# Kernel tuning notes

Measured on AMD Instinct MI355X. Metric: run time of the kernel, lower is better.

The kernel has to match this reference:

```python
import jax, jax.numpy as jnp
import numpy as np

H = 512          # hidden_dim
AA = 21          # aa_num
NF = 6165        # num_features
B, N = 4, 2048   # graphs per batch, nodes per graph
LAMB = 1.0
OUT = 2


def gcn(x, adj, W, b):
    # Kipf GCN with self-loops on a (weighted) dense adjacency [B,n,n].
    n = adj.shape[-1]
    A = adj + jnp.eye(n, dtype=adj.dtype)
    d = jnp.sum(A, axis=-1)
    dinv = jax.lax.rsqrt(jnp.maximum(d, 1e-12))
    xw = x @ W                              # [B,n,Hout]
    msg = dinv[..., :, None] * (A @ (dinv[..., :, None] * xw))
    return msg + b


def hgpsl_pool(x, adj, att):
    # Node information score ||(I - D^-1 A) X||_1 (HGP-SL), top-k ratio 0.5,
    # then structure learning: row-softmax of pairwise attention + lamb*A.
    B_, n, h = x.shape
    d = jnp.sum(adj, axis=-1)
    dinv = 1.0 / jnp.maximum(d, 1.0)
    prop = (dinv[..., :, None] * adj) @ x
    score = jnp.sum(jnp.abs(x - prop), axis=-1)          # [B,n]
    k = n // 2
    _, idx = jax.lax.top_k(score, k)                     # [B,k]
    xk = jnp.take_along_axis(x, idx[:, :, None], axis=1)             # [B,k,h]
    a1 = jnp.take_along_axis(adj, idx[:, :, None], axis=1)           # [B,k,n]
    adjk = jnp.take_along_axis(a1, idx[:, None, :], axis=2)          # [B,k,k]
    # structure learning: e_ij = a^T [x_i || x_j] + lamb * A_ij
    li = xk @ att[:h]                                    # [B,k]
    lj = xk @ att[h:]                                    # [B,k]
    logits = li[:, :, None] + lj[:, None, :] + LAMB * adjk
    new_adj = jax.nn.softmax(logits, axis=-1)            # [B,k,k]
    return xk, new_adj


def readout(x):
    return jnp.concatenate([jnp.max(x, axis=1), jnp.mean(x, axis=1)], axis=-1)


def setup_inputs() -> dict:
    key = jax.random.key(0)
    ks = jax.random.split(key, 16)
    x = jax.random.normal(ks[0], (B, N, NF), dtype=jnp.float32)
    u = jax.random.uniform(ks[1], (B, N, N), dtype=jnp.float32)
    adj = (u < 0.008).astype(jnp.float32)
    adj = jnp.maximum(adj, jnp.swapaxes(adj, 1, 2))
    adj = adj * (1.0 - jnp.eye(N, dtype=jnp.float32))
    def w(k, shape):
        fan = shape[0]
        return jax.random.normal(k, shape, dtype=jnp.float32) / np.sqrt(fan)
    return {
        "x": x, "adj": adj,
        "lin1_W": w(ks[2], (NF - AA, H)), "lin1_b": jnp.zeros((H,), jnp.float32),
        "lin2_W": w(ks[3], (AA, AA)),     "lin2_b": jnp.zeros((AA,), jnp.float32),
        "conv1_W": w(ks[4], (H + AA, H)), "conv1_b": jnp.zeros((H,), jnp.float32),
        "conv2_W": w(ks[5], (H, H)),      "conv2_b": jnp.zeros((H,), jnp.float32),
        "conv3_W": w(ks[6], (H, H)),      "conv3_b": jnp.zeros((H,), jnp.float32),
        "att1": w(ks[7], (2 * H,)), "att2": w(ks[8], (2 * H,)),
        "fc1_W": w(ks[9], (2 * H, H)),    "fc1_b": jnp.zeros((H,), jnp.float32),
        "fc2_W": w(ks[10], (H, H // 2)),  "fc2_b": jnp.zeros((H // 2,), jnp.float32),
        "fc3_W": w(ks[11], (H // 2, OUT)),"fc3_b": jnp.zeros((OUT,), jnp.float32),
    }


def reference(x, adj, lin1_W, lin1_b, lin2_W, lin2_b, conv1_W, conv1_b,
              conv2_W, conv2_b, conv3_W, conv3_b, att1, att2,
              fc1_W, fc1_b, fc2_W, fc2_b, fc3_W, fc3_b):
    relu = jax.nn.relu
    x1 = relu(x[..., AA:] @ lin1_W + lin1_b)   # [B,N,H]
    x2 = relu(x[..., :AA] @ lin2_W + lin2_b)   # [B,N,AA]
    h = jnp.concatenate([x2, x1], axis=-1)     # [B,N,H+AA]
    h = relu(gcn(h, adj, conv1_W, conv1_b))
    h, adj1 = hgpsl_pool(h, adj, att1)         # N -> N/2
    r1 = readout(h)
    h = relu(gcn(h, adj1, conv2_W, conv2_b))
    h, adj2 = hgpsl_pool(h, adj1, att2)        # N/2 -> N/4
    r2 = readout(h)
    h = relu(gcn(h, adj2, conv3_W, conv3_b))
    r3 = readout(h)
    z = relu(r1) + relu(r2) + relu(r3)         # [B,2H]
    z = relu(z @ fc1_W + fc1_b)                # dropout is eval-mode identity
    z = relu(z @ fc2_W + fc2_b)
    return jax.nn.log_softmax(z @ fc3_W + fc3_b, axis=-1)
```

## Files before the change

kernel.cpp:

```cpp
#include <hip/hip_runtime.h>
#include <cstdint>
#include <cstddef>

typedef __bf16 bf16x8 __attribute__((ext_vector_type(8)));
typedef float f32x4 __attribute__((ext_vector_type(4)));

template <int MF>
__global__ __launch_bounds__(256) void gemm_mfma(
    const float* __restrict__ A, long lda, long sAb,
    const __bf16* __restrict__ Bp, long sBpb,
    float* __restrict__ C, long ldc, long sCb,
    int M, int N, int K,
    const float* __restrict__ bias,
    const float* __restrict__ rowscale,
    const float* __restrict__ addm, long sAddb, long ldadd,
    int do_relu)
{
  constexpr int BM = 32 * MF;
  constexpr int CH = MF / 2;
  constexpr int ABUF = MF * 4096;
  __shared__ __align__(16) char smem[2 * ABUF];

  const int bz = blockIdx.z;
  const float* Ab = A + (size_t)bz * sAb;
  const __bf16* Bb = Bp + (size_t)bz * sBpb;
  float* Cb = C + (size_t)bz * sCb;

  int flat = blockIdx.y * gridDim.x + blockIdx.x;
  const int nwg = gridDim.x * gridDim.y;
  if ((nwg & 7) == 0) { const int q = nwg >> 3; flat = (flat & 7) * q + (flat >> 3); }
  const int col0 = (flat / gridDim.y) * 128;
  const int row0 = (flat % gridDim.y) * BM;

  const int t = threadIdx.x;
  const int w = t >> 6, l = t & 63;
  const int l16 = l & 15, lq = l >> 4;
  const int wr = w >> 1, wc = w & 1;
  const int T = K >> 5;

  int aoff[CH]; const float* aptr[CH];
#pragma unroll
  for (int ch = 0; ch < CH; ++ch) {
    const int c = t + ch * 256;
    const int row = c >> 2, oct = c & 3;
    aoff[ch] = (row >> 4) * 1024 + (oct * 16 + (row & 15)) * 16;
    aptr[ch] = Ab + (size_t)(row0 + row) * lda + oct * 8;
  }

  const __bf16* bB[4];
#pragma unroll
  for (int nf = 0; nf < 4; ++nf)
    bB[nf] = Bb + ((size_t)((col0 >> 4) + wc * 4 + nf) * T) * 1024 + l * 8;

  f32x4 acc[MF][4];
#pragma unroll
  for (int i = 0; i < MF; ++i)
#pragma unroll
    for (int j = 0; j < 4; ++j) acc[i][j] = (f32x4){0.f, 0.f, 0.f, 0.f};

  float a0r[CH * 8], a1r[CH * 8];
  bf16x8 b0h[4], b0l[4], b1h[4], b1l[4];

#define GA(dst, K0)                                                         \
  { _Pragma("unroll") for (int ch = 0; ch < CH; ++ch) {                     \
      const float* ap = aptr[ch] + (K0);                                    \
      _Pragma("unroll") for (int i = 0; i < 8; ++i) dst[ch * 8 + i] = ap[i]; } }

#define GB(dh, dl, KT)                                                      \
  { _Pragma("unroll") for (int nf = 0; nf < 4; ++nf) {                      \
      dh[nf] = *(const bf16x8*)(bB[nf] + (size_t)(KT) * 1024);              \
      dl[nf] = *(const bf16x8*)(bB[nf] + (size_t)(KT) * 1024 + 512); } }

#define WA(buf, src)                                                        \
  { char* wb = smem + (buf) * ABUF;                                         \
    _Pragma("unroll") for (int ch = 0; ch < CH; ++ch) {                     \
      bf16x8 vh, vl;                                                        \
      _Pragma("unroll") for (int i = 0; i < 8; ++i) {                       \
        const __bf16 hh = (__bf16)src[ch * 8 + i];                          \
        vh[i] = hh; vl[i] = (__bf16)(src[ch * 8 + i] - (float)hh); }        \
      *(bf16x8*)(wb + aoff[ch]) = vh;                                       \
      *(bf16x8*)(wb + MF * 2048 + aoff[ch]) = vl; } }

#define COMPUTE(buf, bh, bl)                                                \
  { const char* rb = smem + (buf) * ABUF;                                   \
    _Pragma("unroll") for (int mf = 0; mf < MF; ++mf) {                     \
      const int fg = wr * MF + mf;                                          \
      bf16x8 fh = *(const bf16x8*)(rb + fg * 1024 + l * 16);                \
      bf16x8 fl = *(const bf16x8*)(rb + MF * 2048 + fg * 1024 + l * 16);    \
      _Pragma("unroll") for (int nf = 0; nf < 4; ++nf) {                    \
        acc[mf][nf] = __builtin_amdgcn_mfma_f32_16x16x32_bf16(fl, bh[nf], acc[mf][nf], 0, 0, 0); \
        acc[mf][nf] = __builtin_amdgcn_mfma_f32_16x16x32_bf16(fh, bl[nf], acc[mf][nf], 0, 0, 0); \
        acc[mf][nf] = __builtin_amdgcn_mfma_f32_16x16x32_bf16(fh, bh[nf], acc[mf][nf], 0, 0, 0); } } }

  GA(a0r, 0); GB(b0h, b0l, 0);
  if (T > 1) GA(a1r, 32);
  WA(0, a0r);
  __syncthreads();

  int kt = 0;
  for (; kt + 2 <= T; kt += 2) {
    if (kt + 2 < T) GA(a0r, (kt + 2) * 32);
    GB(b1h, b1l, kt + 1);
    COMPUTE(0, b0h, b0l);
    WA(1, a1r);
    __syncthreads();
    if (kt + 3 < T) GA(a1r, (kt + 3) * 32);
    if (kt + 2 < T) GB(b0h, b0l, kt + 2);
    COMPUTE(1, b1h, b1l);
    if (kt + 2 < T) WA(0, a0r);
    __syncthreads();
  }
  if (kt < T) {
    COMPUTE(0, b0h, b0l);
  }
#undef GA
#undef GB
#undef WA
#undef COMPUTE

#pragma unroll
  for (int mf = 0; mf < MF; ++mf) {
#pragma unroll
    for (int r = 0; r < 4; ++r) {
      const int row = row0 + wr * (MF * 16) + mf * 16 + lq * 4 + r;
      const float rs = rowscale ? rowscale[(size_t)bz * M + row] : 1.f;
#pragma unroll
      for (int nf = 0; nf < 4; ++nf) {
        const int col = col0 + wc * 64 + nf * 16 + l16;
        float v = acc[mf][nf][r];
        if (addm) v += addm[(size_t)bz * sAddb + (size_t)row * ldadd + col];
        v *= rs;
        if (bias) v += bias[col];
        if (do_relu) v = fmaxf(v, 0.f);
        Cb[(size_t)row * ldc + col] = v;
      }
    }
  }
}

__global__ __launch_bounds__(64) void pack_b_kernel(
    const float* __restrict__ in, long sInb, int Kin, int Nin,
    __bf16* __restrict__ outP, long sPb, int T)
{
  const int kt = blockIdx.x, nf = blockIdx.y, b = blockIdx.z;
  const int l = threadIdx.x;
  const float* src = in + (size_t)b * sInb;
  const int col = nf * 16 + (l & 15);
  const int k0 = kt * 32 + (l >> 4) * 8;
  bf16x8 vh, vl;
#pragma unroll
  for (int j = 0; j < 8; ++j) {
    const int k = k0 + j;
    const float v = (k < Kin) ? src[(size_t)k * Nin + col] : 0.f;
    const __bf16 h = (__bf16)v;
    vh[j] = h; vl[j] = (__bf16)(v - (float)h);
  }
  __bf16* dst = outP + (size_t)b * sPb + ((size_t)nf * T + kt) * 1024 + l * 8;
  *(bf16x8*)dst = vh;
  *(bf16x8*)(dst + 512) = vl;
}

__global__ void lin2_kernel(const float* __restrict__ x, const float* __restrict__ W,
                            const float* __restrict__ b, float* __restrict__ h)
{
  int id = blockIdx.x * blockDim.x + threadIdx.x;
  if (id >= 4 * 2048 * 21) return;
  int row = id / 21, j = id % 21;
  const float* xr = x + (size_t)row * 6165;
  float acc = b[j];
  for (int i = 0; i < 21; ++i) acc = fmaf(xr[i], W[i * 21 + j], acc);
  h[(size_t)row * 544 + j] = fmaxf(acc, 0.f);
}

__global__ void pad_h_kernel(float* __restrict__ h)
{
  int id = blockIdx.x * blockDim.x + threadIdx.x;
  if (id >= 4 * 2048 * 11) return;
  int row = id / 11, c = 533 + id % 11;
  h[(size_t)row * 544 + c] = 0.f;
}

__global__ __launch_bounds__(256) void degrees_kernel(const float* __restrict__ adj,
                                                      float* __restrict__ dg,
                                                      float* __restrict__ dp)
{
  __shared__ float red[256];
  const int row = blockIdx.x;
  const int t = threadIdx.x;
  const float* ar = adj + (size_t)row * 2048;
  float s = 0.f;
  for (int j = t; j < 2048; j += 256) s += ar[j];
  red[t] = s; __syncthreads();
  for (int off = 128; off > 0; off >>= 1) {
    if (t < off) red[t] += red[t + off];
    __syncthreads();
  }
  if (t == 0) {
    float S = red[0];
    dg[row] = rsqrtf(fmaxf(S + 1.f, 1e-12f));
    dp[row] = 1.f / fmaxf(S, 1.f);
  }
}

__global__ __launch_bounds__(256) void conv1_msg_kernel(
    const float* __restrict__ adj, const float* __restrict__ xw,
    const float* __restrict__ dinv, const float* __restrict__ bias,
    float* __restrict__ out)
{
  __shared__ int nbr[2048];
  __shared__ float nval[2048];
  __shared__ int cnts[256];
  const int b = blockIdx.y, i = blockIdx.x, t = threadIdx.x;
  const float* ar = adj + ((size_t)(b * 2048 + i)) * 2048;
  int myj[8]; float myv[8]; int mc = 0;
  const int j0 = t * 8;
#pragma unroll
  for (int q = 0; q < 8; ++q) {
    float v = ar[j0 + q];
    if (v != 0.f) { myj[mc] = j0 + q; myv[mc] = v; ++mc; }
  }
  cnts[t] = mc; __syncthreads();
  for (int off = 1; off < 256; off <<= 1) {
    int v = cnts[t]; int add = (t >= off) ? cnts[t - off] : 0;
    __syncthreads();
    cnts[t] = v + add; __syncthreads();
  }
  const int base = cnts[t] - mc;
  const int total = cnts[255];
  for (int q = 0; q < mc; ++q) { nbr[base + q] = myj[q]; nval[base + q] = myv[q]; }
  __syncthreads();

  const float* xwb = xw + (size_t)b * 2048 * 512;
  const float* dv = dinv + b * 2048;
  float acc0 = 0.f, acc1 = 0.f;
  for (int n = 0; n < total; ++n) {
    const int j = nbr[n];
    const float w = nval[n] * dv[j];
    const float* xr = xwb + (size_t)j * 512;
    acc0 = fmaf(w, xr[t], acc0);
    acc1 = fmaf(w, xr[t + 256], acc1);
  }
  const float di = dv[i];
  const float* xi = xwb + (size_t)i * 512;
  acc0 = fmaf(di, xi[t], acc0);
  acc1 = fmaf(di, xi[t + 256], acc1);
  float* orow = out + ((size_t)(b * 2048 + i)) * 512;
  orow[t]       = fmaxf(di * acc0 + bias[t], 0.f);
  orow[t + 256] = fmaxf(di * acc1 + bias[t + 256], 0.f);
}

__global__ __launch_bounds__(256) void pool1_score_kernel(
    const float* __restrict__ adj, const float* __restrict__ h1,
    const float* __restrict__ dpool, float* __restrict__ score)
{
  __shared__ int nbr[2048];
  __shared__ float nval[2048];
  __shared__ int cnts[256];
  __shared__ float red[256];
  const int b = blockIdx.y, i = blockIdx.x, t = threadIdx.x;
  const float* ar = adj + ((size_t)(b * 2048 + i)) * 2048;
  int myj[8]; float myv[8]; int mc = 0;
  const int j0 = t * 8;
#pragma unroll
  for (int q = 0; q < 8; ++q) {
    float v = ar[j0 + q];
    if (v != 0.f) { myj[mc] = j0 + q; myv[mc] = v; ++mc; }
  }
  cnts[t] = mc; __syncthreads();
  for (int off = 1; off < 256; off <<= 1) {
    int v = cnts[t]; int add = (t >= off) ? cnts[t - off] : 0;
    __syncthreads();
    cnts[t] = v + add; __syncthreads();
  }
  const int base = cnts[t] - mc;
  const int total = cnts[255];
  for (int q = 0; q < mc; ++q) { nbr[base + q] = myj[q]; nval[base + q] = myv[q]; }
  __syncthreads();

  const float* hb = h1 + (size_t)b * 2048 * 512;
  float acc0 = 0.f, acc1 = 0.f;
  for (int n = 0; n < total; ++n) {
    const int j = nbr[n];
    const float w = nval[n];
    const float* xr = hb + (size_t)j * 512;
    acc0 = fmaf(w, xr[t], acc0);
    acc1 = fmaf(w, xr[t + 256], acc1);
  }
  const float dpi = dpool[b * 2048 + i];
  const float* hi = hb + (size_t)i * 512;
  float part = fabsf(hi[t] - dpi * acc0) + fabsf(hi[t + 256] - dpi * acc1);
  red[t] = part; __syncthreads();
  for (int off = 128; off > 0; off >>= 1) {
    if (t < off) red[t] += red[t + off];
    __syncthreads();
  }
  if (t == 0) score[b * 2048 + i] = red[0];
}

__global__ __launch_bounds__(1024) void topk_kernel(
    const float* __restrict__ score, int* __restrict__ idx_out, int n, int k)
{
  __shared__ unsigned long long key[2048];
  const unsigned b = blockIdx.x, t = threadIdx.x;
  const unsigned bd = blockDim.x;
  for (unsigned i = t; i < (unsigned)n; i += bd) {
    unsigned u = __float_as_uint(score[(size_t)b * n + i]);
    key[i] = ((unsigned long long)u << 32) | (unsigned)(~i);
  }
  __syncthreads();
  for (unsigned size = 2; size <= (unsigned)n; size <<= 1) {
    for (unsigned stride = size >> 1; stride > 0; stride >>= 1) {
      const unsigned i = (t / stride) * (stride * 2) + (t % stride);
      const unsigned ixj = i + stride;
      const bool up = ((i & size) == 0);
      unsigned long long a = key[i], c = key[ixj];
      if (up ? (a < c) : (a > c)) { key[i] = c; key[ixj] = a; }
      __syncthreads();
    }
  }
  const unsigned my = ~(unsigned)(key[t] & 0xFFFFFFFFull);
  __syncthreads();
  unsigned* arr = (unsigned*)key;
  arr[t] = my;
  __syncthreads();
  for (unsigned size = 2; size <= (unsigned)k; size <<= 1) {
    for (unsigned stride = size >> 1; stride > 0; stride >>= 1) {
      if (t < (unsigned)k / 2) {
        const unsigned i = (t / stride) * (stride * 2) + (t % stride);
        const unsigned ixj = i + stride;
        const bool up = ((i & size) == 0);
        unsigned a = arr[i], c = arr[ixj];
        if (up ? (a > c) : (a < c)) { arr[i] = c; arr[ixj] = a; }
      }
      __syncthreads();
    }
  }
  idx_out[(size_t)b * k + t] = (int)arr[t];
}

__global__ __launch_bounds__(256) void gather_li_kernel(
    const float* __restrict__ X, int src_n,
    const int* __restrict__ idx, int k,
    const float* __restrict__ att,
    float* __restrict__ xk, float* __restrict__ li, float* __restrict__ lj)
{
  __shared__ float redA[256], redB[256];
  const int b = blockIdx.y, r = blockIdx.x, t = threadIdx.x;
  const int g = idx[(size_t)b * k + r];
  const float* src = X + ((size_t)(b * src_n + g)) * 512;
  float* dst = xk + ((size_t)(b * k + r)) * 512;
  const float v0 = src[t], v1 = src[t + 256];
  dst[t] = v0; dst[t + 256] = v1;
  redA[t] = v0 * att[t] + v1 * att[t + 256];
  redB[t] = v0 * att[512 + t] + v1 * att[512 + t + 256];
  __syncthreads();
  for (int off = 128; off > 0; off >>= 1) {
    if (t < off) { redA[t] += redA[t + off]; redB[t] += redB[t + off]; }
    __syncthreads();
  }
  if (t == 0) { li[(size_t)b * k + r] = redA[0]; lj[(size_t)b * k + r] = redB[0]; }
}

__global__ __launch_bounds__(256) void slearn_kernel(
    const float* __restrict__ Asrc, int src_n,
    const int* __restrict__ idx, int k,
    const float* __restrict__ li, const float* __restrict__ lj,
    float* __restrict__ adj_out, float* __restrict__ dg, float* __restrict__ dp)
{
  __shared__ int gidx[1024];
  __shared__ float ljv[1024];
  __shared__ float lg[1024];
  __shared__ float red[256];
  const int b = blockIdx.y, r = blockIdx.x, t = threadIdx.x;
  for (int j = t; j < k; j += 256) { gidx[j] = idx[(size_t)b * k + j]; ljv[j] = lj[(size_t)b * k + j]; }
  __syncthreads();
  const int gi = gidx[r];
  const float lir = li[(size_t)b * k + r];
  const float* ar = Asrc + ((size_t)(b * src_n + gi)) * src_n;
  float mx = -3.4e38f;
  for (int j = t; j < k; j += 256) {
    float v = lir + ljv[j] + ar[gidx[j]];
    lg[j] = v; mx = fmaxf(mx, v);
  }
  red[t] = mx; __syncthreads();
  for (int off = 128; off > 0; off >>= 1) {
    if (t < off) red[t] = fmaxf(red[t], red[t + off]);
    __syncthreads();
  }
  const float m = red[0]; __syncthreads();
  float sm = 0.f;
  for (int j = t; j < k; j += 256) { float e = expf(lg[j] - m); lg[j] = e; sm += e; }
  red[t] = sm; __syncthreads();
  for (int off = 128; off > 0; off >>= 1) {
    if (t < off) red[t] += red[t + off];
    __syncthreads();
  }
  const float s = red[0]; __syncthreads();
  const float inv = 1.f / s;
  float ps = 0.f;
  float* orow = adj_out + ((size_t)(b * k + r)) * k;
  for (int j = t; j < k; j += 256) { float p = lg[j] * inv; orow[j] = p; ps += p; }
  red[t] = ps; __syncthreads();
  for (int off = 128; off > 0; off >>= 1) {
    if (t < off) red[t] += red[t + off];
    __syncthreads();
  }
  if (t == 0) {
    float S = red[0];
    dg[(size_t)b * k + r] = rsqrtf(fmaxf(S + 1.f, 1e-12f));
    dp[(size_t)b * k + r] = 1.f / fmaxf(S, 1.f);
  }
}

__global__ __launch_bounds__(512) void absdiff_kernel(
    const float* __restrict__ X, const float* __restrict__ P, float* __restrict__ score)
{
  __shared__ float red[512];
  const int row = blockIdx.x, t = threadIdx.x;
  float d = fabsf(X[(size_t)row * 512 + t] - P[(size_t)row * 512 + t]);
  red[t] = d; __syncthreads();
  for (int off = 256; off > 0; off >>= 1) {
    if (t < off) red[t] += red[t + off];
    __syncthreads();
  }
  if (t == 0) score[row] = red[0];
}

__global__ __launch_bounds__(512) void readout_part_kernel(
    const float* __restrict__ X, int nrows, int chunk_rows,
    float* __restrict__ partM, float* __restrict__ partS)
{
  const int b = blockIdx.x, chunk = blockIdx.y, c = threadIdx.x;
  const float* xb = X + ((size_t)b * nrows + (size_t)chunk * chunk_rows) * 512;
  float mx = -3.4e38f, sm = 0.f;
  for (int r = 0; r < chunk_rows; ++r) {
    float v = xb[(size_t)r * 512 + c];
    mx = fmaxf(mx, v); sm += v;
  }
  const size_t o = ((size_t)(b * gridDim.y + chunk)) * 512 + c;
  partM[o] = mx; partS[o] = sm;
}

__global__ __launch_bounds__(512) void readout_comb_kernel(
    const float* __restrict__ partM, const float* __restrict__ partS,
    int nchunks, int nrows, float* __restrict__ out)
{
  const int b = blockIdx.x, c = threadIdx.x;
  float mx = -3.4e38f, sm = 0.f;
  for (int q = 0; q < nchunks; ++q) {
    const size_t o = ((size_t)(b * nchunks + q)) * 512 + c;
    mx = fmaxf(mx, partM[o]); sm += partS[o];
  }
  out[(size_t)b * 1024 + c] = mx;
  out[(size_t)b * 1024 + 512 + c] = sm / (float)nrows;
}

__global__ __launch_bounds__(512) void final_mlp_kernel(
    const float* __restrict__ r1, const float* __restrict__ r2, const float* __restrict__ r3,
    const float* __restrict__ fc1W, const float* __restrict__ fc1b,
    const float* __restrict__ fc2W, const float* __restrict__ fc2b,
    const float* __restrict__ fc3W, const float* __restrict__ fc3b,
    float* __restrict__ out)
{
  __shared__ float z[1024];
  __shared__ float z1[512];
  __shared__ float z2[256];
  __shared__ float l[2];
  const int b = blockIdx.x, t = threadIdx.x;
  for (int c = t; c < 1024; c += 512)
    z[c] = fmaxf(r1[(size_t)b * 1024 + c], 0.f) + fmaxf(r2[(size_t)b * 1024 + c], 0.f)
         + fmaxf(r3[(size_t)b * 1024 + c], 0.f);
  __syncthreads();
  {
    float acc = fc1b[t];
    for (int i = 0; i < 1024; ++i) acc = fmaf(z[i], fc1W[(size_t)i * 512 + t], acc);
    z1[t] = fmaxf(acc, 0.f);
  }
  __syncthreads();
  if (t < 256) {
    float acc = fc2b[t];
    for (int i = 0; i < 512; ++i) acc = fmaf(z1[i], fc2W[(size_t)i * 256 + t], acc);
    z2[t] = fmaxf(acc, 0.f);
  }
  __syncthreads();
  if (t < 2) {
    float acc = fc3b[t];
    for (int i = 0; i < 256; ++i) acc = fmaf(z2[i], fc3W[(size_t)i * 2 + t], acc);
    l[t] = acc;
  }
  __syncthreads();
  if (t == 0) {
    float m = fmaxf(l[0], l[1]);
    float ls = m + logf(expf(l[0] - m) + expf(l[1] - m));
    out[b * 2 + 0] = l[0] - ls;
    out[b * 2 + 1] = l[1] - ls;
  }
}

extern "C" void kernel_launch(void* const* d_in, const int* in_sizes, int n_in,
                              void* d_out, int out_size, void* d_ws, size_t ws_size,
                              hipStream_t stream)
{
  (void)in_sizes; (void)n_in; (void)out_size; (void)ws_size;
  const float* x       = (const float*)d_in[0];
  const float* adj     = (const float*)d_in[1];
  const float* lin1_W  = (const float*)d_in[2];
  const float* lin1_b  = (const float*)d_in[3];
  const float* lin2_W  = (const float*)d_in[4];
  const float* lin2_b  = (const float*)d_in[5];
  const float* conv1_W = (const float*)d_in[6];
  const float* conv1_b = (const float*)d_in[7];
  const float* conv2_W = (const float*)d_in[8];
  const float* conv2_b = (const float*)d_in[9];
  const float* conv3_W = (const float*)d_in[10];
  const float* conv3_b = (const float*)d_in[11];
  const float* att1    = (const float*)d_in[12];
  const float* att2    = (const float*)d_in[13];
  const float* fc1_W   = (const float*)d_in[14];
  const float* fc1_b   = (const float*)d_in[15];
  const float* fc2_W   = (const float*)d_in[16];
  const float* fc2_b   = (const float*)d_in[17];
  const float* fc3_W   = (const float*)d_in[18];
  const float* fc3_b   = (const float*)d_in[19];
  float* ws  = (float*)d_ws;
  float* out = (float*)d_out;

  float* h     = ws + 0;
  float* adj1  = ws + 0;
  float* xw    = ws + 4456448;
  float* prop2 = xw;
  float* xk2   = ws + 4456448 + 2097152;
  float* adj2  = ws + 4456448 + 3145728;
  float* h1    = ws + 8650752;
  float* xk1   = ws + 12845056;
  float* xw3   = xk1;
  float* h3    = ws + 12845056 + 1048576;
  float* xw2   = ws + 14942208;
  float* h2    = ws + 17039360;
  float* S     = ws + 19136512;
  float* dinv_g1 = S;
  float* dinv_p1 = S + 8192;
  float* score1  = S + 16384;
  int*   idx1    = (int*)(S + 24576);
  float* li1     = S + 28672;
  float* lj1     = S + 32768;
  float* r1      = S + 36864;
  float* dinv_g2 = S + 40960;
  float* dinv_p2 = S + 45056;
  float* score2  = S + 49152;
  int*   idx2    = (int*)(S + 53248);
  float* li2     = S + 55296;
  float* lj2     = S + 57344;
  float* r2      = S + 59392;
  float* dinv_g3 = S + 63488;
  float* dinv_p3 = S + 65536;
  float* r3      = S + 67584;

  float* partM = ws + 4718592;
  float* partS = ws + 4718592 + 32768;

  __bf16* l1P  = (__bf16*)(ws + 8650752);
  __bf16* c1P  = (__bf16*)(ws + 12845056);
  __bf16* c2P  = (__bf16*)(ws + 17039360);
  __bf16* c3P  = (__bf16*)(ws + 4456448);
  __bf16* xw2P = (__bf16*)(ws + 12845056);
  __bf16* h2P  = (__bf16*)(ws + 8650752);
  __bf16* xw3P = (__bf16*)(ws + 10747904);

  pack_b_kernel<<<dim3(192, 32, 1), 64, 0, stream>>>(lin1_W, 0, 6144, 512, l1P, 0, 192);
  pack_b_kernel<<<dim3(17, 32, 1), 64, 0, stream>>>(conv1_W, 0, 533, 512, c1P, 0, 17);
  pack_b_kernel<<<dim3(16, 32, 1), 64, 0, stream>>>(conv2_W, 0, 512, 512, c2P, 0, 16);
  lin2_kernel<<<(4 * 2048 * 21 + 255) / 256, 256, 0, stream>>>(x, lin2_W, lin2_b, h);
  pad_h_kernel<<<(4 * 2048 * 11 + 255) / 256, 256, 0, stream>>>(h);
  gemm_mfma<2><<<dim3(4, 128, 1), 256, 0, stream>>>(x + 21, 6165, 0, l1P, 0,
      h + 21, 544, 0, 8192, 512, 6144, lin1_b, nullptr, nullptr, 0, 0, 1);
  degrees_kernel<<<8192, 256, 0, stream>>>(adj, dinv_g1, dinv_p1);
  gemm_mfma<2><<<dim3(4, 128, 1), 256, 0, stream>>>(h, 544, 0, c1P, 0,
      xw, 512, 0, 8192, 512, 544, nullptr, nullptr, nullptr, 0, 0, 0);
  conv1_msg_kernel<<<dim3(2048, 4), 256, 0, stream>>>(adj, xw, dinv_g1, conv1_b, h1);
  pool1_score_kernel<<<dim3(2048, 4), 256, 0, stream>>>(adj, h1, dinv_p1, score1);
  topk_kernel<<<4, 1024, 0, stream>>>(score1, idx1, 2048, 1024);
  gather_li_kernel<<<dim3(1024, 4), 256, 0, stream>>>(h1, 2048, idx1, 1024, att1, xk1, li1, lj1);
  slearn_kernel<<<dim3(1024, 4), 256, 0, stream>>>(adj, 2048, idx1, 1024, li1, lj1, adj1, dinv_g2, dinv_p2);
  readout_part_kernel<<<dim3(4, 16), 512, 0, stream>>>(xk1, 1024, 64, partM, partS);
  readout_comb_kernel<<<4, 512, 0, stream>>>(partM, partS, 16, 1024, r1);
  gemm_mfma<2><<<dim3(4, 64, 1), 256, 0, stream>>>(xk1, 512, 0, c2P, 0,
      xw2, 512, 0, 4096, 512, 512, nullptr, dinv_g2, nullptr, 0, 0, 0);
  pack_b_kernel<<<dim3(32, 32, 4), 64, 0, stream>>>(xw2, 524288, 1024, 512, xw2P, 1048576, 32);
  gemm_mfma<2><<<dim3(4, 16, 4), 256, 0, stream>>>(adj1, 1024, 1048576, xw2P, 1048576,
      h2, 512, 524288, 1024, 512, 1024, conv2_b, dinv_g2, xw2, 524288, 512, 1);
  pack_b_kernel<<<dim3(32, 32, 4), 64, 0, stream>>>(h2, 524288, 1024, 512, h2P, 1048576, 32);
  gemm_mfma<2><<<dim3(4, 16, 4), 256, 0, stream>>>(adj1, 1024, 1048576, h2P, 1048576,
      prop2, 512, 524288, 1024, 512, 1024, nullptr, dinv_p2, nullptr, 0, 0, 0);
  absdiff_kernel<<<4096, 512, 0, stream>>>(h2, prop2, score2);
  pack_b_kernel<<<dim3(16, 32, 1), 64, 0, stream>>>(conv3_W, 0, 512, 512, c3P, 0, 16);
  topk_kernel<<<4, 512, 0, stream>>>(score2, idx2, 1024, 512);
  gather_li_kernel<<<dim3(512, 4), 256, 0, stream>>>(h2, 1024, idx2, 512, att2, xk2, li2, lj2);
  slearn_kernel<<<dim3(512, 4), 256, 0, stream>>>(adj1, 1024, idx2, 512, li2, lj2, adj2, dinv_g3, dinv_p3);
  readout_part_kernel<<<dim3(4, 16), 512, 0, stream>>>(xk2, 512, 32, partM, partS);
  readout_comb_kernel<<<4, 512, 0, stream>>>(partM, partS, 16, 512, r2);
  gemm_mfma<2><<<dim3(4, 32, 1), 256, 0, stream>>>(xk2, 512, 0, c3P, 0,
      xw3, 512, 0, 2048, 512, 512, nullptr, dinv_g3, nullptr, 0, 0, 0);
  pack_b_kernel<<<dim3(16, 32, 4), 64, 0, stream>>>(xw3, 262144, 512, 512, xw3P, 524288, 16);
  gemm_mfma<2><<<dim3(4, 8, 4), 256, 0, stream>>>(adj2, 512, 262144, xw3P, 524288,
      h3, 512, 262144, 512, 512, 512, conv3_b, dinv_g3, xw3, 262144, 512, 1);
  readout_part_kernel<<<dim3(4, 16), 512, 0, stream>>>(h3, 512, 32, partM, partS);
  readout_comb_kernel<<<4, 512, 0, stream>>>(partM, partS, 16, 512, r3);
  final_mlp_kernel<<<4, 512, 0, stream>>>(r1, r2, r3, fc1_W, fc1_b, fc2_W, fc2_b,
                                          fc3_W, fc3_b, out);
}
```

Before: 788.4 us.

## Load A fragments directly to registers, drop LDS staging, triple-buffer prefetch

The GEMM kernel no longer stages the fp32 A tile through shared memory. Each lane now loads its own MFMA fragment rows straight from global memory and splits them into bf16 hi/lo in registers. The two-stage LDS double buffer and its __syncthreads barriers give way to a three-deep register prefetch of A and B tiles. This removes LDS traffic and block-wide synchronisation, but each wave redundantly loads A rows that the other column-wave also needs. It also uses uncoalesced 32-byte-per-lane global reads and adds register pressure that may lower occupancy.

```diff
diff --git a/kernel.cpp b/kernel.cpp
--- a/kernel.cpp
+++ b/kernel.cpp
@@ -17,9 +17,6 @@
     int do_relu)
 {
   constexpr int BM = 32 * MF;
-  constexpr int CH = MF / 2;
-  constexpr int ABUF = MF * 4096;
-  __shared__ __align__(16) char smem[2 * ABUF];
 
   const int bz = blockIdx.z;
   const float* Ab = A + (size_t)bz * sAb;
@@ -38,14 +35,10 @@
   const int wr = w >> 1, wc = w & 1;
   const int T = K >> 5;
 
-  int aoff[CH]; const float* aptr[CH];
-#pragma unroll
-  for (int ch = 0; ch < CH; ++ch) {
-    const int c = t + ch * 256;
-    const int row = c >> 2, oct = c & 3;
-    aoff[ch] = (row >> 4) * 1024 + (oct * 16 + (row & 15)) * 16;
-    aptr[ch] = Ab + (size_t)(row0 + row) * lda + oct * 8;
-  }
+  const float* aptr[MF];
+#pragma unroll
+  for (int mf = 0; mf < MF; ++mf)
+    aptr[mf] = Ab + (size_t)(row0 + (wr * MF + mf) * 16 + l16) * lda + lq * 8;
 
   const __bf16* bB[4];
 #pragma unroll
@@ -58,64 +51,48 @@
 #pragma unroll
     for (int j = 0; j < 4; ++j) acc[i][j] = (f32x4){0.f, 0.f, 0.f, 0.f};
 
-  float a0r[CH * 8], a1r[CH * 8];
-  bf16x8 b0h[4], b0l[4], b1h[4], b1l[4];
-
-#define GA(dst, K0)                                                         \
-  { _Pragma("unroll") for (int ch = 0; ch < CH; ++ch) {                     \
-      const float* ap = aptr[ch] + (K0);                                    \
-      _Pragma("unroll") for (int i = 0; i < 8; ++i) dst[ch * 8 + i] = ap[i]; } }
+  float a0[MF][8], a1[MF][8], a2[MF][8];
+  bf16x8 b0h[4], b0l[4], b1h[4], b1l[4], b2h[4], b2l[4];
+
+#define GA(dst, KT)                                                         \
+  { _Pragma("unroll") for (int mf = 0; mf < MF; ++mf) {                     \
+      const float* ap = aptr[mf] + (size_t)(KT) * 32;                       \
+      _Pragma("unroll") for (int i = 0; i < 8; ++i) dst[mf][i] = ap[i]; } }
 
 #define GB(dh, dl, KT)                                                      \
   { _Pragma("unroll") for (int nf = 0; nf < 4; ++nf) {                      \
       dh[nf] = *(const bf16x8*)(bB[nf] + (size_t)(KT) * 1024);              \
       dl[nf] = *(const bf16x8*)(bB[nf] + (size_t)(KT) * 1024 + 512); } }
 
-#define WA(buf, src)                                                        \
-  { char* wb = smem + (buf) * ABUF;                                         \
-    _Pragma("unroll") for (int ch = 0; ch < CH; ++ch) {                     \
-      bf16x8 vh, vl;                                                        \
+#define COMPUTE(a, bh, bl)                                                  \
+  { _Pragma("unroll") for (int mf = 0; mf < MF; ++mf) {                     \
+      bf16x8 fh, fl;                                                        \
       _Pragma("unroll") for (int i = 0; i < 8; ++i) {                       \
-        const __bf16 hh = (__bf16)src[ch * 8 + i];                          \
-        vh[i] = hh; vl[i] = (__bf16)(src[ch * 8 + i] - (float)hh); }        \
-      *(bf16x8*)(wb + aoff[ch]) = vh;                                       \
-      *(bf16x8*)(wb + MF * 2048 + aoff[ch]) = vl; } }
-
-#define COMPUTE(buf, bh, bl)                                                \
-  { const char* rb = smem + (buf) * ABUF;                                   \
-    _Pragma("unroll") for (int mf = 0; mf < MF; ++mf) {                     \
-      const int fg = wr * MF + mf;                                          \
-      bf16x8 fh = *(const bf16x8*)(rb + fg * 1024 + l * 16);                \
-      bf16x8 fl = *(const bf16x8*)(rb + MF * 2048 + fg * 1024 + l * 16);    \
+        const __bf16 hh = (__bf16)a[mf][i];                                 \
+        fh[i] = hh; fl[i] = (__bf16)(a[mf][i] - (float)hh); }               \
       _Pragma("unroll") for (int nf = 0; nf < 4; ++nf) {                    \
         acc[mf][nf] = __builtin_amdgcn_mfma_f32_16x16x32_bf16(fl, bh[nf], acc[mf][nf], 0, 0, 0); \
         acc[mf][nf] = __builtin_amdgcn_mfma_f32_16x16x32_bf16(fh, bl[nf], acc[mf][nf], 0, 0, 0); \
         acc[mf][nf] = __builtin_amdgcn_mfma_f32_16x16x32_bf16(fh, bh[nf], acc[mf][nf], 0, 0, 0); } } }
 
-  GA(a0r, 0); GB(b0h, b0l, 0);
-  if (T > 1) GA(a1r, 32);
-  WA(0, a0r);
-  __syncthreads();
+  GA(a0, 0); GB(b0h, b0l, 0);
+  if (T > 1) { GA(a1, 1); GB(b1h, b1l, 1); }
+  if (T > 2) { GA(a2, 2); GB(b2h, b2l, 2); }
 
   int kt = 0;
-  for (; kt + 2 <= T; kt += 2) {
-    if (kt + 2 < T) GA(a0r, (kt + 2) * 32);
-    GB(b1h, b1l, kt + 1);
-    COMPUTE(0, b0h, b0l);
-    WA(1, a1r);
-    __syncthreads();
-    if (kt + 3 < T) GA(a1r, (kt + 3) * 32);
-    if (kt + 2 < T) GB(b0h, b0l, kt + 2);
-    COMPUTE(1, b1h, b1l);
-    if (kt + 2 < T) WA(0, a0r);
-    __syncthreads();
-  }
-  if (kt < T) {
-    COMPUTE(0, b0h, b0l);
-  }
+  for (; kt + 3 <= T; kt += 3) {
+    COMPUTE(a0, b0h, b0l);
+    if (kt + 3 < T) { GA(a0, kt + 3); GB(b0h, b0l, kt + 3); }
+    COMPUTE(a1, b1h, b1l);
+    if (kt + 4 < T) { GA(a1, kt + 4); GB(b1h, b1l, kt + 4); }
+    COMPUTE(a2, b2h, b2l);
+    if (kt + 5 < T) { GA(a2, kt + 5); GB(b2h, b2l, kt + 5); }
+  }
+  if (kt < T)     COMPUTE(a0, b0h, b0l);
+  if (kt + 1 < T) COMPUTE(a1, b1h, b1l);
+  if (kt + 2 < T) COMPUTE(a2, b2h, b2l);
 #undef GA
 #undef GB
-#undef WA
 #undef COMPUTE
 
 #pragma unroll
```

New measurement: 830.4 us. 1.05x slower.

## Split GEMM K loop across two wave groups with LDS reduction

Applied to the files above, without the earlier changes.

The MFMA GEMM now launches 512 threads per block. Two groups of four waves each handle half of the K tiles, then combine their accumulators through shared memory before the epilogue. This raises the wave count per tile and per CU, which can hide memory latency better on the long-K lin1 GEMM. The tile-to-block mapping also changes to column-fastest order. The cost is an extra LDS reduction, more syncs, and redundant clamped B loads when T is odd.

```diff
diff --git a/kernel.cpp b/kernel.cpp
--- a/kernel.cpp
+++ b/kernel.cpp
@@ -5,8 +5,7 @@
 typedef __bf16 bf16x8 __attribute__((ext_vector_type(8)));
 typedef float f32x4 __attribute__((ext_vector_type(4)));
 
-template <int MF>
-__global__ __launch_bounds__(256) void gemm_mfma(
+__global__ __launch_bounds__(512) void gemm_mfma(
     const float* __restrict__ A, long lda, long sAb,
     const __bf16* __restrict__ Bp, long sBpb,
     float* __restrict__ C, long ldc, long sCb,
@@ -16,10 +15,7 @@
     const float* __restrict__ addm, long sAddb, long ldadd,
     int do_relu)
 {
-  constexpr int BM = 32 * MF;
-  constexpr int CH = MF / 2;
-  constexpr int ABUF = MF * 4096;
-  __shared__ __align__(16) char smem[2 * ABUF];
+  __shared__ __align__(16) char smem[2 * 16384];
 
   const int bz = blockIdx.z;
   const float* Ab = A + (size_t)bz * sAb;
@@ -29,88 +25,89 @@
   int flat = blockIdx.y * gridDim.x + blockIdx.x;
   const int nwg = gridDim.x * gridDim.y;
   if ((nwg & 7) == 0) { const int q = nwg >> 3; flat = (flat & 7) * q + (flat >> 3); }
-  const int col0 = (flat / gridDim.y) * 128;
-  const int row0 = (flat % gridDim.y) * BM;
+  const int col0 = (flat % gridDim.x) * 128;
+  const int row0 = (flat / gridDim.x) * 64;
 
   const int t = threadIdx.x;
   const int w = t >> 6, l = t & 63;
   const int l16 = l & 15, lq = l >> 4;
-  const int wr = w >> 1, wc = w & 1;
+  const int ksg = w >> 2;
+  const int wr = (w >> 1) & 1, wc = w & 1;
+  const int wloc = w & 3;
   const int T = K >> 5;
-
-  int aoff[CH]; const float* aptr[CH];
-#pragma unroll
-  for (int ch = 0; ch < CH; ++ch) {
-    const int c = t + ch * 256;
-    const int row = c >> 2, oct = c & 3;
-    aoff[ch] = (row >> 4) * 1024 + (oct * 16 + (row & 15)) * 16;
-    aptr[ch] = Ab + (size_t)(row0 + row) * lda + oct * 8;
-  }
+  const int T0 = (T + 1) >> 1;
+
+  const int sgs = t >> 8, ts = t & 255;
+  const int s_row = ts >> 2, s_oct = ts & 3;
+  const int a_off = (s_row >> 4) * 1024 + (s_oct * 16 + (s_row & 15)) * 16;
+  const float* aStage = Ab + (size_t)(row0 + s_row) * lda + s_oct * 8;
 
   const __bf16* bB[4];
 #pragma unroll
   for (int nf = 0; nf < 4; ++nf)
     bB[nf] = Bb + ((size_t)((col0 >> 4) + wc * 4 + nf) * T) * 1024 + l * 8;
 
-  f32x4 acc[MF][4];
-#pragma unroll
-  for (int i = 0; i < MF; ++i)
+  f32x4 acc[2][4];
+#pragma unroll
+  for (int i = 0; i < 2; ++i)
 #pragma unroll
     for (int j = 0; j < 4; ++j) acc[i][j] = (f32x4){0.f, 0.f, 0.f, 0.f};
 
-  float a0r[CH * 8], a1r[CH * 8];
+  float a0[8], a1[8];
   bf16x8 b0h[4], b0l[4], b1h[4], b1l[4];
 
-#define GA(dst, K0)                                                         \
-  { _Pragma("unroll") for (int ch = 0; ch < CH; ++ch) {                     \
-      const float* ap = aptr[ch] + (K0);                                    \
-      _Pragma("unroll") for (int i = 0; i < 8; ++i) dst[ch * 8 + i] = ap[i]; } }
-
-#define GB(dh, dl, KT)                                                      \
-  { _Pragma("unroll") for (int nf = 0; nf < 4; ++nf) {                      \
-      dh[nf] = *(const bf16x8*)(bB[nf] + (size_t)(KT) * 1024);              \
-      dl[nf] = *(const bf16x8*)(bB[nf] + (size_t)(KT) * 1024 + 512); } }
+#define GA(dst, I)                                                          \
+  { const int gg = sgs * T0 + (I);                                          \
+    if (gg < T) { const float* ap = aStage + (size_t)gg * 32;               \
+      _Pragma("unroll") for (int i2 = 0; i2 < 8; ++i2) dst[i2] = ap[i2];    \
+    } else {                                                                \
+      _Pragma("unroll") for (int i2 = 0; i2 < 8; ++i2) dst[i2] = 0.f; } }
+
+#define GB(dh, dl, I)                                                       \
+  { const int gg = min(ksg * T0 + (I), T - 1);                              \
+    _Pragma("unroll") for (int nf = 0; nf < 4; ++nf) {                      \
+      dh[nf] = *(const bf16x8*)(bB[nf] + (size_t)gg * 1024);                \
+      dl[nf] = *(const bf16x8*)(bB[nf] + (size_t)gg * 1024 + 512); } }
 
 #define WA(buf, src)                                                        \
-  { char* wb = smem + (buf) * ABUF;                                         \
-    _Pragma("unroll") for (int ch = 0; ch < CH; ++ch) {                     \
-      bf16x8 vh, vl;                                                        \
-      _Pragma("unroll") for (int i = 0; i < 8; ++i) {                       \
-        const __bf16 hh = (__bf16)src[ch * 8 + i];                          \
-        vh[i] = hh; vl[i] = (__bf16)(src[ch * 8 + i] - (float)hh); }        \
-      *(bf16x8*)(wb + aoff[ch]) = vh;                                       \
-      *(bf16x8*)(wb + MF * 2048 + aoff[ch]) = vl; } }
+  { char* wb = smem + (buf) * 16384 + sgs * 8192;                           \
+    bf16x8 vh, vl;                                                          \
+    _Pragma("unroll") for (int i2 = 0; i2 < 8; ++i2) {                      \
+      const __bf16 hh = (__bf16)src[i2];                                    \
+      vh[i2] = hh; vl[i2] = (__bf16)(src[i2] - (float)hh); }                \
+    *(bf16x8*)(wb + a_off) = vh;                                            \
+    *(bf16x8*)(wb + 4096 + a_off) = vl; }
 
 #define COMPUTE(buf, bh, bl)                                                \
-  { const char* rb = smem + (buf) * ABUF;                                   \
-    _Pragma("unroll") for (int mf = 0; mf < MF; ++mf) {                     \
-      const int fg = wr * MF + mf;                                          \
+  { const char* rb = smem + (buf) * 16384 + ksg * 8192;                     \
+    _Pragma("unroll") for (int mf = 0; mf < 2; ++mf) {                      \
+      const int fg = wr * 2 + mf;                                           \
       bf16x8 fh = *(const bf16x8*)(rb + fg * 1024 + l * 16);                \
-      bf16x8 fl = *(const bf16x8*)(rb + MF * 2048 + fg * 1024 + l * 16);    \
+      bf16x8 fl = *(const bf16x8*)(rb + 4096 + fg * 1024 + l * 16);         \
       _Pragma("unroll") for (int nf = 0; nf < 4; ++nf) {                    \
         acc[mf][nf] = __builtin_amdgcn_mfma_f32_16x16x32_bf16(fl, bh[nf], acc[mf][nf], 0, 0, 0); \
         acc[mf][nf] = __builtin_amdgcn_mfma_f32_16x16x32_bf16(fh, bl[nf], acc[mf][nf], 0, 0, 0); \
         acc[mf][nf] = __builtin_amdgcn_mfma_f32_16x16x32_bf16(fh, bh[nf], acc[mf][nf], 0, 0, 0); } } }
 
-  GA(a0r, 0); GB(b0h, b0l, 0);
-  if (T > 1) GA(a1r, 32);
-  WA(0, a0r);
+  GA(a0, 0); GB(b0h, b0l, 0);
+  if (T0 > 1) GA(a1, 1);
+  WA(0, a0);
   __syncthreads();
 
   int kt = 0;
-  for (; kt + 2 <= T; kt += 2) {
-    if (kt + 2 < T) GA(a0r, (kt + 2) * 32);
+  for (; kt + 2 <= T0; kt += 2) {
+    if (kt + 2 < T0) GA(a0, kt + 2);
     GB(b1h, b1l, kt + 1);
     COMPUTE(0, b0h, b0l);
-    WA(1, a1r);
-    __syncthreads();
-    if (kt + 3 < T) GA(a1r, (kt + 3) * 32);
-    if (kt + 2 < T) GB(b0h, b0l, kt + 2);
+    WA(1, a1);
+    __syncthreads();
+    if (kt + 3 < T0) GA(a1, kt + 3);
+    if (kt + 2 < T0) GB(b0h, b0l, kt + 2);
     COMPUTE(1, b1h, b1l);
-    if (kt + 2 < T) WA(0, a0r);
-    __syncthreads();
-  }
-  if (kt < T) {
+    if (kt + 2 < T0) WA(0, a0);
+    __syncthreads();
+  }
+  if (kt < T0) {
     COMPUTE(0, b0h, b0l);
   }
 #undef GA
@@ -118,21 +115,40 @@
 #undef WA
 #undef COMPUTE
 
-#pragma unroll
-  for (int mf = 0; mf < MF; ++mf) {
-#pragma unroll
-    for (int r = 0; r < 4; ++r) {
-      const int row = row0 + wr * (MF * 16) + mf * 16 + lq * 4 + r;
-      const float rs = rowscale ? rowscale[(size_t)bz * M + row] : 1.f;
+  __syncthreads();
+  f32x4* red4 = (f32x4*)smem;
+  if (ksg == 1) {
+#pragma unroll
+    for (int mf = 0; mf < 2; ++mf)
+#pragma unroll
+      for (int nf = 0; nf < 4; ++nf)
+        red4[(wloc * 64 + l) * 8 + ((mf * 4 + nf) ^ (l & 7))] = acc[mf][nf];
+  }
+  __syncthreads();
+  if (ksg == 0) {
+#pragma unroll
+    for (int mf = 0; mf < 2; ++mf)
 #pragma unroll
       for (int nf = 0; nf < 4; ++nf) {
-        const int col = col0 + wc * 64 + nf * 16 + l16;
-        float v = acc[mf][nf][r];
-        if (addm) v += addm[(size_t)bz * sAddb + (size_t)row * ldadd + col];
-        v *= rs;
-        if (bias) v += bias[col];
-        if (do_relu) v = fmaxf(v, 0.f);
-        Cb[(size_t)row * ldc + col] = v;
+        const f32x4 v = red4[(wloc * 64 + l) * 8 + ((mf * 4 + nf) ^ (l & 7))];
+        acc[mf][nf] = acc[mf][nf] + v;
+      }
+#pragma unroll
+    for (int mf = 0; mf < 2; ++mf) {
+#pragma unroll
+      for (int r = 0; r < 4; ++r) {
+        const int row = row0 + wr * 32 + mf * 16 + lq * 4 + r;
+        const float rs = rowscale ? rowscale[(size_t)bz * M + row] : 1.f;
+#pragma unroll
+        for (int nf = 0; nf < 4; ++nf) {
+          const int col = col0 + wc * 64 + nf * 16 + l16;
+          float v = acc[mf][nf][r];
+          if (addm) v += addm[(size_t)bz * sAddb + (size_t)row * ldadd + col];
+          v *= rs;
+          if (bias) v += bias[col];
+          if (do_relu) v = fmaxf(v, 0.f);
+          Cb[(size_t)row * ldc + col] = v;
+        }
       }
     }
   }
@@ -572,10 +588,10 @@
   pack_b_kernel<<<dim3(16, 32, 1), 64, 0, stream>>>(conv2_W, 0, 512, 512, c2P, 0, 16);
   lin2_kernel<<<(4 * 2048 * 21 + 255) / 256, 256, 0, stream>>>(x, lin2_W, lin2_b, h);
   pad_h_kernel<<<(4 * 2048 * 11 + 255) / 256, 256, 0, stream>>>(h);
-  gemm_mfma<2><<<dim3(4, 128, 1), 256, 0, stream>>>(x + 21, 6165, 0, l1P, 0,
+  gemm_mfma<<<dim3(4, 128, 1), 512, 0, stream>>>(x + 21, 6165, 0, l1P, 0,
       h + 21, 544, 0, 8192, 512, 6144, lin1_b, nullptr, nullptr, 0, 0, 1);
   degrees_kernel<<<8192, 256, 0, stream>>>(adj, dinv_g1, dinv_p1);
-  gemm_mfma<2><<<dim3(4, 128, 1), 256, 0, stream>>>(h, 544, 0, c1P, 0,
+  gemm_mfma<<<dim3(4, 128, 1), 512, 0, stream>>>(h, 544, 0, c1P, 0,
       xw, 512, 0, 8192, 512, 544, nullptr, nullptr, nullptr, 0, 0, 0);
   conv1_msg_kernel<<<dim3(2048, 4), 256, 0, stream>>>(adj, xw, dinv_g1, conv1_b, h1);
   pool1_score_kernel<<<dim3(2048, 4), 256, 0, stream>>>(adj, h1, dinv_p1, score1);
@@ -584,13 +600,13 @@
   slearn_kernel<<<dim3(1024, 4), 256, 0, stream>>>(adj, 2048, idx1, 1024, li1, lj1, adj1, dinv_g2, dinv_p2);
   readout_part_kernel<<<dim3(4, 16), 512, 0, stream>>>(xk1, 1024, 64, partM, partS);
   readout_comb_kernel<<<4, 512, 0, stream>>>(partM, partS, 16, 1024, r1);
-  gemm_mfma<2><<<dim3(4, 64, 1), 256, 0, stream>>>(xk1, 512, 0, c2P, 0,
+  gemm_mfma<<<dim3(4, 64, 1), 512, 0, stream>>>(xk1, 512, 0, c2P, 0,
       xw2, 512, 0, 4096, 512, 512, nullptr, dinv_g2, nullptr, 0, 0, 0);
   pack_b_kernel<<<dim3(32, 32, 4), 64, 0, stream>>>(xw2, 524288, 1024, 512, xw2P, 1048576, 32);
-  gemm_mfma<2><<<dim3(4, 16, 4), 256, 0, stream>>>(adj1, 1024, 1048576, xw2P, 1048576,
+  gemm_mfma<<<dim3(4, 16, 4), 512, 0, stream>>>(adj1, 1024, 1048576, xw2P, 1048576,
       h2, 512, 524288, 1024, 512, 1024, conv2_b, dinv_g2, xw2, 524288, 512, 1);
   pack_b_kernel<<<dim3(32, 32, 4), 64, 0, stream>>>(h2, 524288, 1024, 512, h2P, 1048576, 32);
-  gemm_mfma<2><<<dim3(4, 16, 4), 256, 0, stream>>>(adj1, 1024, 1048576, h2P, 1048576,
+  gemm_mfma<<<dim3(4, 16, 4), 512, 0, stream>>>(adj1, 1024, 1048576, h2P, 1048576,
       prop2, 512, 524288, 1024, 512, 1024, nullptr, dinv_p2, nullptr, 0, 0, 0);
   absdiff_kernel<<<4096, 512, 0, stream>>>(h2, prop2, score2);
   pack_b_kernel<<<dim3(16, 32, 1), 64, 0, stream>>>(conv3_W, 0, 512, 512, c3P, 0, 16);
@@ -599,10 +615,10 @@
   slearn_kernel<<<dim3(512, 4), 256, 0, stream>>>(adj1, 1024, idx2, 512, li2, lj2, adj2, dinv_g3, dinv_p3);
   readout_part_kernel<<<dim3(4, 16), 512, 0, stream>>>(xk2, 512, 32, partM, partS);
   readout_comb_kernel<<<4, 512, 0, stream>>>(partM, partS, 16, 512, r2);
-  gemm_mfma<2><<<dim3(4, 32, 1), 256, 0, stream>>>(xk2, 512, 0, c3P, 0,
+  gemm_mfma<<<dim3(4, 32, 1), 512, 0, stream>>>(xk2, 512, 0, c3P, 0,
       xw3, 512, 0, 2048, 512, 512, nullptr, dinv_g3, nullptr, 0, 0, 0);
   pack_b_kernel<<<dim3(16, 32, 4), 64, 0, stream>>>(xw3, 262144, 512, 512, xw3P, 524288, 16);
-  gemm_mfma<2><<<dim3(4, 8, 4), 256, 0, stream>>>(adj2, 512, 262144, xw3P, 524288,
+  gemm_mfma<<<dim3(4, 8, 4), 512, 0, stream>>>(adj2, 512, 262144, xw3P, 524288,
       h3, 512, 262144, 512, 512, 512, conv3_b, dinv_g3, xw3, 262144, 512, 1);
   readout_part_kernel<<<dim3(4, 16), 512, 0, stream>>>(h3, 512, 32, partM, partS);
   readout_comb_kernel<<<4, 512, 0, stream>>>(partM, partS, 16, 512, r3);
```

Result: no change. 773.4 us (-1.9%).

## Add split-K to MFMA GEMM with separate combine epilogue kernel

Applied to the files above, without the earlier changes.

Adds a split-K mode to the MFMA GEMM. Each split writes a partial result to workspace, and a new combine kernel sums the two partials and applies the addm, rowscale, bias and relu epilogue. It is enabled for the lin1, conv1 and both conv2 adjacency GEMMs to raise the number of workgroups and improve CU utilization. The tile mapping changes from column-major to row-major over flat block ids, and the conv2 weight packing moves later. In exchange it adds partial-buffer traffic and extra kernel launches, and it reuses workspace regions that must not alias live data.

```diff
diff --git a/kernel.cpp b/kernel.cpp
--- a/kernel.cpp
+++ b/kernel.cpp
@@ -14,29 +14,34 @@
     const float* __restrict__ bias,
     const float* __restrict__ rowscale,
     const float* __restrict__ addm, long sAddb, long ldadd,
-    int do_relu)
+    int do_relu, int nsplit, long sSplit)
 {
   constexpr int BM = 32 * MF;
   constexpr int CH = MF / 2;
   constexpr int ABUF = MF * 4096;
   __shared__ __align__(16) char smem[2 * ABUF];
 
-  const int bz = blockIdx.z;
-  const float* Ab = A + (size_t)bz * sAb;
+  const int bzz = blockIdx.z;
+  const int bz = bzz / nsplit, ks = bzz % nsplit;
+  const int T_all = K >> 5;
+  const int Tk = (T_all + nsplit - 1) / nsplit;
+  const int t0 = ks * Tk;
+  const int T = min(Tk, T_all - t0);
+
+  const float* Ab = A + (size_t)bz * sAb + (size_t)t0 * 32;
   const __bf16* Bb = Bp + (size_t)bz * sBpb;
-  float* Cb = C + (size_t)bz * sCb;
+  float* Cb = C + (size_t)bz * sCb + (size_t)ks * sSplit;
 
   int flat = blockIdx.y * gridDim.x + blockIdx.x;
   const int nwg = gridDim.x * gridDim.y;
   if ((nwg & 7) == 0) { const int q = nwg >> 3; flat = (flat & 7) * q + (flat >> 3); }
-  const int col0 = (flat / gridDim.y) * 128;
-  const int row0 = (flat % gridDim.y) * BM;
+  const int col0 = (flat % gridDim.x) * 128;
+  const int row0 = (flat / gridDim.x) * BM;
 
   const int t = threadIdx.x;
   const int w = t >> 6, l = t & 63;
   const int l16 = l & 15, lq = l >> 4;
   const int wr = w >> 1, wc = w & 1;
-  const int T = K >> 5;
 
   int aoff[CH]; const float* aptr[CH];
 #pragma unroll
@@ -50,7 +55,7 @@
   const __bf16* bB[4];
 #pragma unroll
   for (int nf = 0; nf < 4; ++nf)
-    bB[nf] = Bb + ((size_t)((col0 >> 4) + wc * 4 + nf) * T) * 1024 + l * 8;
+    bB[nf] = Bb + ((size_t)((col0 >> 4) + wc * 4 + nf) * T_all + t0) * 1024 + l * 8;
 
   f32x4 acc[MF][4];
 #pragma unroll
@@ -135,6 +140,27 @@
         Cb[(size_t)row * ldc + col] = v;
       }
     }
+  }
+}
+
+__global__ __launch_bounds__(256) void combine_kernel(
+    const float* __restrict__ P0, long sPb, long sSplit,
+    float* __restrict__ C, long ldc, long sCb, int M, int N,
+    const float* __restrict__ bias, const float* __restrict__ rowscale,
+    const float* __restrict__ addm, long sAddb, long ldadd, int do_relu)
+{
+  const int b = blockIdx.y;
+  const size_t total = (size_t)M * N;
+  const float* p = P0 + (size_t)b * sPb;
+  for (size_t idx = (size_t)blockIdx.x * 256 + threadIdx.x; idx < total;
+       idx += (size_t)gridDim.x * 256) {
+    const int r = (int)(idx / N), c = (int)(idx % N);
+    float v = p[idx] + p[idx + sSplit];
+    if (addm) v += addm[(size_t)b * sAddb + (size_t)r * ldadd + c];
+    if (rowscale) v *= rowscale[(size_t)b * M + r];
+    if (bias) v += bias[c];
+    if (do_relu) v = fmaxf(v, 0.f);
+    C[(size_t)b * sCb + (size_t)r * ldc + c] = v;
   }
 }
 
@@ -567,16 +593,28 @@
   __bf16* h2P  = (__bf16*)(ws + 8650752);
   __bf16* xw3P = (__bf16*)(ws + 10747904);
 
+  float* Plin1 = ws + 4456448;
+  const long sLin1 = 8667136;
+  float* Pxw   = ws + 8650752;
+  const long sXw = 6291456;
+  float* P12   = ws + 8650752;
+  const long s12 = 2097152;
+  float* P13   = ws + 12845056;
+  const long s13 = 2097152;
+
   pack_b_kernel<<<dim3(192, 32, 1), 64, 0, stream>>>(lin1_W, 0, 6144, 512, l1P, 0, 192);
   pack_b_kernel<<<dim3(17, 32, 1), 64, 0, stream>>>(conv1_W, 0, 533, 512, c1P, 0, 17);
-  pack_b_kernel<<<dim3(16, 32, 1), 64, 0, stream>>>(conv2_W, 0, 512, 512, c2P, 0, 16);
   lin2_kernel<<<(4 * 2048 * 21 + 255) / 256, 256, 0, stream>>>(x, lin2_W, lin2_b, h);
   pad_h_kernel<<<(4 * 2048 * 11 + 255) / 256, 256, 0, stream>>>(h);
-  gemm_mfma<2><<<dim3(4, 128, 1), 256, 0, stream>>>(x + 21, 6165, 0, l1P, 0,
-      h + 21, 544, 0, 8192, 512, 6144, lin1_b, nullptr, nullptr, 0, 0, 1);
+  gemm_mfma<2><<<dim3(4, 128, 2), 256, 0, stream>>>(x + 21, 6165, 0, l1P, 0,
+      Plin1, 512, 0, 8192, 512, 6144, nullptr, nullptr, nullptr, 0, 0, 0, 2, sLin1);
+  combine_kernel<<<dim3(2048, 1), 256, 0, stream>>>(Plin1, 0, sLin1,
+      h + 21, 544, 0, 8192, 512, lin1_b, nullptr, nullptr, 0, 0, 1);
   degrees_kernel<<<8192, 256, 0, stream>>>(adj, dinv_g1, dinv_p1);
-  gemm_mfma<2><<<dim3(4, 128, 1), 256, 0, stream>>>(h, 544, 0, c1P, 0,
-      xw, 512, 0, 8192, 512, 544, nullptr, nullptr, nullptr, 0, 0, 0);
+  gemm_mfma<2><<<dim3(4, 128, 2), 256, 0, stream>>>(h, 544, 0, c1P, 0,
+      Pxw, 512, 0, 8192, 512, 544, nullptr, nullptr, nullptr, 0, 0, 0, 2, sXw);
+  combine_kernel<<<dim3(2048, 1), 256, 0, stream>>>(Pxw, 0, sXw,
+      xw, 512, 0, 8192, 512, nullptr, nullptr, nullptr, 0, 0, 0);
   conv1_msg_kernel<<<dim3(2048, 4), 256, 0, stream>>>(adj, xw, dinv_g1, conv1_b, h1);
   pool1_score_kernel<<<dim3(2048, 4), 256, 0, stream>>>(adj, h1, dinv_p1, score1);
   topk_kernel<<<4, 1024, 0, stream>>>(score1, idx1, 2048, 1024);
@@ -584,14 +622,19 @@
   slearn_kernel<<<dim3(1024, 4), 256, 0, stream>>>(adj, 2048, idx1, 1024, li1, lj1, adj1, dinv_g2, dinv_p2);
   readout_part_kernel<<<dim3(4, 16), 512, 0, stream>>>(xk1, 1024, 64, partM, partS);
   readout_comb_kernel<<<4, 512, 0, stream>>>(partM, partS, 16, 1024, r1);
+  pack_b_kernel<<<dim3(16, 32, 1), 64, 0, stream>>>(conv2_W, 0, 512, 512, c2P, 0, 16);
   gemm_mfma<2><<<dim3(4, 64, 1), 256, 0, stream>>>(xk1, 512, 0, c2P, 0,
-      xw2, 512, 0, 4096, 512, 512, nullptr, dinv_g2, nullptr, 0, 0, 0);
+      xw2, 512, 0, 4096, 512, 512, nullptr, dinv_g2, nullptr, 0, 0, 0, 1, 0);
   pack_b_kernel<<<dim3(32, 32, 4), 64, 0, stream>>>(xw2, 524288, 1024, 512, xw2P, 1048576, 32);
-  gemm_mfma<2><<<dim3(4, 16, 4), 256, 0, stream>>>(adj1, 1024, 1048576, xw2P, 1048576,
-      h2, 512, 524288, 1024, 512, 1024, conv2_b, dinv_g2, xw2, 524288, 512, 1);
+  gemm_mfma<2><<<dim3(4, 16, 8), 256, 0, stream>>>(adj1, 1024, 1048576, xw2P, 1048576,
+      P12, 512, 524288, 1024, 512, 1024, nullptr, nullptr, nullptr, 0, 0, 0, 2, s12);
+  combine_kernel<<<dim3(1024, 4), 256, 0, stream>>>(P12, 524288, s12,
+      h2, 512, 524288, 1024, 512, conv2_b, dinv_g2, xw2, 524288, 512, 1);
   pack_b_kernel<<<dim3(32, 32, 4), 64, 0, stream>>>(h2, 524288, 1024, 512, h2P, 1048576, 32);
-  gemm_mfma<2><<<dim3(4, 16, 4), 256, 0, stream>>>(adj1, 1024, 1048576, h2P, 1048576,
-      prop2, 512, 524288, 1024, 512, 1024, nullptr, dinv_p2, nullptr, 0, 0, 0);
+  gemm_mfma<2><<<dim3(4, 16, 8), 256, 0, stream>>>(adj1, 1024, 1048576, h2P, 1048576,
+      P13, 512, 524288, 1024, 512, 1024, nullptr, nullptr, nullptr, 0, 0, 0, 2, s13);
+  combine_kernel<<<dim3(1024, 4), 256, 0, stream>>>(P13, 524288, s13,
+      prop2, 512, 524288, 1024, 512, nullptr, dinv_p2, nullptr, 0, 0, 0);
   absdiff_kernel<<<4096, 512, 0, stream>>>(h2, prop2, score2);
   pack_b_kernel<<<dim3(16, 32, 1), 64, 0, stream>>>(conv3_W, 0, 512, 512, c3P, 0, 16);
   topk_kernel<<<4, 512, 0, stream>>>(score2, idx2, 1024, 512);
@@ -600,10 +643,10 @@
   readout_part_kernel<<<dim3(4, 16), 512, 0, stream>>>(xk2, 512, 32, partM, partS);
   readout_comb_kernel<<<4, 512, 0, stream>>>(partM, partS, 16, 512, r2);
   gemm_mfma<2><<<dim3(4, 32, 1), 256, 0, stream>>>(xk2, 512, 0, c3P, 0,
-      xw3, 512, 0, 2048, 512, 512, nullptr, dinv_g3, nullptr, 0, 0, 0);
+      xw3, 512, 0, 2048, 512, 512, nullptr, dinv_g3, nullptr, 0, 0, 0, 1, 0);
   pack_b_kernel<<<dim3(16, 32, 4), 64, 0, stream>>>(xw3, 262144, 512, 512, xw3P, 524288, 16);
   gemm_mfma<2><<<dim3(4, 8, 4), 256, 0, stream>>>(adj2, 512, 262144, xw3P, 524288,
-      h3, 512, 262144, 512, 512, 512, conv3_b, dinv_g3, xw3, 262144, 512, 1);
+      h3, 512, 262144, 512, 512, 512, conv3_b, dinv_g3, xw3, 262144, 512, 1, 1, 0);
   readout_part_kernel<<<dim3(4, 16), 512, 0, stream>>>(h3, 512, 32, partM, partS);
   readout_comb_kernel<<<4, 512, 0, stream>>>(partM, partS, 16, 512, r3);
   final_mlp_kernel<<<4, 512, 0, stream>>>(r1, r2, r3, fc1_W, fc1_b, fc2_W, fc2_b,
```

Result: slower. 805.0 us (+2.1%).
